# Performance work log

Hardware: AMD Instinct MI355X
Metric: run time of the kernel (lower is better)

Reference implementation:

```python
import jax, jax.numpy as jnp
import numpy as np
from jax import lax

B, T, I, H, N = 8192, 100, 24, 64, 8  # batch, seq_len, input_size, hidden_size, hidden_neurons
H2 = 2 * H


def setup_inputs() -> dict:
    key = jax.random.key(0)
    ks = iter(jax.random.split(key, 80))
    d = {"input_seq": jax.random.normal(next(ks), (B, T, I), jnp.float32)}
    def triple(name, shape):
        d[name + "_mu"] = 0.1 * jax.random.normal(next(ks), shape, jnp.float32)
        d[name + "_rho"] = -6.0 + 0.1 * jax.random.normal(next(ks), shape, jnp.float32)
        d[name + "_eps"] = jax.random.normal(next(ks), shape, jnp.float32)
    # BayesianLSTM params: weight_ih (in, 4H), weight_hh (H, 4H), bias (4H,)
    triple("l1_wih", (I, 4 * H)); triple("l1_whh", (H, 4 * H)); triple("l1_b", (4 * H,))
    triple("l2_wih", (H, 4 * H2)); triple("l2_whh", (H2, 4 * H2)); triple("l2_b", (4 * H2,))
    # BayesianLinear params: weight (out, in), bias (out,)
    triple("fc1_w", (N, H2)); triple("fc1_b", (N,))
    triple("fc2_w", (N, N)); triple("fc2_b", (N,))
    triple("out_w", (1, N)); triple("out_b", (1,))
    return d


def _sample(mu, rho, eps):
    # blitz reparameterization: sigma = log1p(exp(rho))
    return mu + jnp.log1p(jnp.exp(rho)) * eps


def _lstm(x, wih, whh, b):
    # x: [B, T, in]; returns full hidden sequence [B, T, Hn]; gate order i,f,g,o
    Hn = whh.shape[0]
    xg = jnp.einsum('bti,ig->btg', x, wih) + b  # precompute input projection
    def step(carry, xg_t):
        h, c = carry
        gates = xg_t + h @ whh
        i, f, g, o = jnp.split(gates, 4, axis=-1)
        c = jax.nn.sigmoid(f) * c + jax.nn.sigmoid(i) * jnp.tanh(g)
        h = jax.nn.sigmoid(o) * jnp.tanh(c)
        return (h, c), h
    h0 = jnp.zeros((x.shape[0], Hn), x.dtype)
    _, hs = lax.scan(step, (h0, h0), jnp.swapaxes(xg, 0, 1))
    return jnp.swapaxes(hs, 0, 1)


def _forward(input_seq,
             l1_wih_mu, l1_wih_rho, l1_wih_eps, l1_whh_mu, l1_whh_rho, l1_whh_eps,
             l1_b_mu, l1_b_rho, l1_b_eps,
             l2_wih_mu, l2_wih_rho, l2_wih_eps, l2_whh_mu, l2_whh_rho, l2_whh_eps,
             l2_b_mu, l2_b_rho, l2_b_eps,
             fc1_w_mu, fc1_w_rho, fc1_w_eps, fc1_b_mu, fc1_b_rho, fc1_b_eps,
             fc2_w_mu, fc2_w_rho, fc2_w_eps, fc2_b_mu, fc2_b_rho, fc2_b_eps,
             out_w_mu, out_w_rho, out_w_eps, out_b_mu, out_b_rho, out_b_eps):
    w1i = _sample(l1_wih_mu, l1_wih_rho, l1_wih_eps)
    w1h = _sample(l1_whh_mu, l1_whh_rho, l1_whh_eps)
    b1 = _sample(l1_b_mu, l1_b_rho, l1_b_eps)
    w2i = _sample(l2_wih_mu, l2_wih_rho, l2_wih_eps)
    w2h = _sample(l2_whh_mu, l2_whh_rho, l2_whh_eps)
    b2 = _sample(l2_b_mu, l2_b_rho, l2_b_eps)
    fc1w = _sample(fc1_w_mu, fc1_w_rho, fc1_w_eps); fc1b = _sample(fc1_b_mu, fc1_b_rho, fc1_b_eps)
    fc2w = _sample(fc2_w_mu, fc2_w_rho, fc2_w_eps); fc2b = _sample(fc2_b_mu, fc2_b_rho, fc2_b_eps)
    outw = _sample(out_w_mu, out_w_rho, out_w_eps); outb = _sample(out_b_mu, out_b_rho, out_b_eps)

    h1 = _lstm(input_seq, w1i, w1h, b1)      # [B, T, H]
    h2 = _lstm(h1, w2i, w2h, b2)             # [B, T, 2H]
    out = h2[:, -1, :]                       # [B, 2H]
    x = jax.nn.relu(out @ fc1w.T + fc1b)
    x = jax.nn.relu(x @ fc2w.T + fc2b)
    y = x @ outw.T + outb                    # [B, 1]
    return y.reshape(-1)


def reference(input_seq,
              l1_wih_mu, l1_wih_rho, l1_wih_eps, l1_whh_mu, l1_whh_rho, l1_whh_eps,
              l1_b_mu, l1_b_rho, l1_b_eps,
              l2_wih_mu, l2_wih_rho, l2_wih_eps, l2_whh_mu, l2_whh_rho, l2_whh_eps,
              l2_b_mu, l2_b_rho, l2_b_eps,
              fc1_w_mu, fc1_w_rho, fc1_w_eps, fc1_b_mu, fc1_b_rho, fc1_b_eps,
              fc2_w_mu, fc2_w_rho, fc2_w_eps, fc2_b_mu, fc2_b_rho, fc2_b_eps,
              out_w_mu, out_w_rho, out_w_eps, out_b_mu, out_b_rho, out_b_eps):
    return _forward(input_seq,
                    l1_wih_mu, l1_wih_rho, l1_wih_eps, l1_whh_mu, l1_whh_rho, l1_whh_eps,
                    l1_b_mu, l1_b_rho, l1_b_eps,
                    l2_wih_mu, l2_wih_rho, l2_wih_eps, l2_whh_mu, l2_whh_rho, l2_whh_eps,
                    l2_b_mu, l2_b_rho, l2_b_eps,
                    fc1_w_mu, fc1_w_rho, fc1_w_eps, fc1_b_mu, fc1_b_rho, fc1_b_eps,
                    fc2_w_mu, fc2_w_rho, fc2_w_eps, fc2_b_mu, fc2_b_rho, fc2_b_eps,
                    out_w_mu, out_w_rho, out_w_eps, out_b_mu, out_b_rho, out_b_eps)
```

## Files before the change

kernel.cpp:

```cpp
#include <hip/hip_runtime.h>
#include <math.h>


typedef __attribute__((ext_vector_type(8))) short short8;
typedef __attribute__((ext_vector_type(4))) float f32x4;

#define MFMA16(a, b, c) __builtin_amdgcn_mfma_f32_16x16x32_bf16((a), (b), (c), 0, 0, 0)

#define WS_W1G_OFF 196608
#define WS_WF_OFF  245760

struct SampParams {
  const float* w1i[3]; const float* w1h[3]; const float* b1[3];
  const float* w2i[3]; const float* w2h[3]; const float* b2[3];
  const float* f1w[3]; const float* f1b[3];
  const float* f2w[3]; const float* f2b[3];
  const float* ow[3];  const float* ob[3];
  short* W2S; short* W1G; float* WF;
};

struct LstmParams {
  const float* input;
  const short* W2S; const short* W1G; const float* WF;
  float* out;
};

__device__ __forceinline__ float samp(const float* const q[3], int idx) {
  return q[0][idx] + log1pf(expf(q[1][idx])) * q[2][idx];
}

__device__ __forceinline__ short f2bf(float f) {
  unsigned u = __float_as_uint(f);
  unsigned r = (u + 0x7FFFu + ((u >> 16) & 1u)) >> 16;
  return (short)r;
}

__device__ __forceinline__ float sigf(float x) {
  return __builtin_amdgcn_rcpf(1.0f + __builtin_amdgcn_exp2f(-1.44269504f * x));
}
__device__ __forceinline__ float tanhf_(float x) {
  return 1.0f - 2.0f * __builtin_amdgcn_rcpf(1.0f + __builtin_amdgcn_exp2f(2.88539008f * x));
}

__global__ __launch_bounds__(256) void sample_kernel(SampParams p)
{
  int i = blockIdx.x * 256 + threadIdx.x;
  if (i < 12288) {
    int tid = i & 511, gg = (i >> 9) & 3, kk = i >> 11;
    int quad = (tid >> 4) & 3, col = tid & 15, v0 = (tid >> 6) * 16;
    int c = gg * 128 + v0 + col;
    short8 v;
#pragma unroll
    for (int j = 0; j < 8; ++j) {
      int k = kk * 32 + quad * 8 + j;
      float x = (k < 64) ? samp(p.w2i, k * 512 + c) : samp(p.w2h, (k - 64) * 512 + c);
      v[j] = f2bf(x);
    }
    *(short8*)&p.W2S[i * 8] = v;
  } else if (i < 15360) {
    int u = i - 12288;
    int slice = u >> 8, n = u & 255;
    int k0 = (slice >> 2) * 32 + (slice & 3) * 8;
    short8 v;
#pragma unroll
    for (int j = 0; j < 8; ++j) {
      int k = k0 + j;
      float x = 0.0f;
      if (k < 24)       x = samp(p.w1i, k * 256 + n);
      else if (k >= 32) x = samp(p.w1h, (k - 32) * 256 + n);
      v[j] = f2bf(x);
    }
    *(short8*)&p.W1G[u * 8] = v;
  } else if (i < 17241) {
    int u = i - 15360;
    float x;
    if (u < 256)       x = samp(p.b1,  u);
    else if (u < 768)  x = samp(p.b2,  u - 256);
    else if (u < 1792) x = samp(p.f1w, u - 768);
    else if (u < 1856) x = samp(p.f2w, u - 1792);
    else if (u < 1864) x = samp(p.f1b, u - 1856);
    else if (u < 1872) x = samp(p.f2b, u - 1864);
    else if (u < 1880) x = samp(p.ow,  u - 1872);
    else               x = samp(p.ob,  0);
    p.WF[u] = x;
  }
}


__global__ __launch_bounds__(512, 2)
void blstm_kernel(LstmParams p)
{
  __shared__ __align__(16) unsigned char pool[79872];
  short* const W1L = (short*)pool;
  short* const A1b = (short*)(pool + 49152);
  short* const A2b = (short*)(pool + 62464);

  const int tid  = threadIdx.x;
  const int w    = tid >> 6;
  const int l    = tid & 63;
  const int quad = l >> 4;
  const int col  = l & 15;
  const int b0   = blockIdx.x * 32;

  const int wq = w & 3;
  const int mh = w >> 2;
  const int v0 = w * 16;

  const short8* const W2v = (const short8*)p.W2S;
  short8 w2r[24];
#pragma unroll
  for (int f = 0; f < 24; ++f) w2r[f] = W2v[f * 512 + tid];

#pragma unroll
  for (int r = 0; r < 6; ++r) {
    short8 v = *(const short8*)&p.W1G[(r * 512 + tid) * 8];
    *(short8*)&W1L[(r * 512 + tid) * 8] = v;
  }

  float b1v[4], b2v[4];
#pragma unroll
  for (int g = 0; g < 4; ++g) b1v[g] = p.WF[g * 64 + wq * 16 + col];
#pragma unroll
  for (int g = 0; g < 4; ++g) b2v[g] = p.WF[256 + g * 128 + v0 + col];

  for (int i = tid; i < 6656; i += 512) A1b[i] = 0;
  for (int i = tid; i < 8704; i += 512) A2b[i] = 0;
  __syncthreads();

  int xr = 0, xi = 0;
  const float* xptr = p.input;
  if (tid < 384) {
    int e = tid * 2; xr = e / 24; xi = e - xr * 24;
    const float* base = p.input + (size_t)(b0 + xr) * 2400 + xi;
    float2 xv = *(const float2*)base;
    unsigned pk = (unsigned)(unsigned short)f2bf(xv.x)
                | ((unsigned)(unsigned short)f2bf(xv.y) << 16);
    *(unsigned*)&A1b[xr * 104 + xi] = pk;
    xptr = base + 24;
  }
  __syncthreads();

  f32x4 c1 = {0.f, 0.f, 0.f, 0.f};
  f32x4 c2[2]; c2[0] = c1; c2[1] = c1;
  float hf2[2][4];

  const int a1rd = (mh * 16 + col) * 104;

  for (int j = 0; j <= 100; ++j) {
    const int pb = j & 1;
    const short* const A1r = A1b + pb * 3328;
    const short* const A2r = A2b + pb * 4352;
    short* const A1w = A1b + (pb ^ 1) * 3328;
    short* const A2w = A2b + (pb ^ 1) * 4352;

    const bool do_x = (j <= 98) && (tid < 384);
    float2 xv;
    if (do_x) xv = *(const float2*)xptr;

    short8 aA0 = *(const short8*)&A1r[a1rd +      quad * 8];
    short8 aA1 = *(const short8*)&A1r[a1rd + 32 + quad * 8];
    short8 aA2 = *(const short8*)&A1r[a1rd + 64 + quad * 8];
    f32x4 g1[4];
#pragma unroll
    for (int g = 0; g < 4; ++g) {
      f32x4 acc = (f32x4){b1v[g], b1v[g], b1v[g], b1v[g]};
      acc = MFMA16(aA0, *(const short8*)&W1L[(((0 * 4 + quad) << 8) + g * 64 + wq * 16 + col) * 8], acc);
      acc = MFMA16(aA1, *(const short8*)&W1L[(((1 * 4 + quad) << 8) + g * 64 + wq * 16 + col) * 8], acc);
      acc = MFMA16(aA2, *(const short8*)&W1L[(((2 * 4 + quad) << 8) + g * 64 + wq * 16 + col) * 8], acc);
      g1[g] = acc;
    }

    {
      int u = wq * 16 + col;
#pragma unroll
      for (int i = 0; i < 4; ++i) {
        float iv = sigf(g1[0][i]);
        float fv = sigf(g1[1][i]);
        float gv = tanhf_(g1[2][i]);
        float ov = sigf(g1[3][i]);
        float cn = fv * c1[i] + iv * gv;
        c1[i] = cn;
        A1w[(mh * 16 + quad * 4 + i) * 104 + 32 + u] = f2bf(ov * tanhf_(cn));
      }
    }
    if (do_x) {
      unsigned pk = (unsigned)(unsigned short)f2bf(xv.x)
                  | ((unsigned)(unsigned short)f2bf(xv.y) << 16);
      *(unsigned*)&A1w[xr * 104 + xi] = pk;
    }

    f32x4 g2[2][4];
#pragma unroll
    for (int g = 0; g < 4; ++g) {
      g2[0][g] = (f32x4){b2v[g], b2v[g], b2v[g], b2v[g]};
      g2[1][g] = g2[0][g];
    }
#pragma unroll
    for (int kk = 0; kk < 6; ++kk) {
      short8 a0, a1f;
      if (kk < 2) {
        a0  = *(const short8*)&A1r[      col  * 104 + 32 + kk * 32 + quad * 8];
        a1f = *(const short8*)&A1r[(16 + col) * 104 + 32 + kk * 32 + quad * 8];
      } else {
        int o = (kk - 2) * 32 + quad * 8;
        a0  = *(const short8*)&A2r[      col  * 136 + o];
        a1f = *(const short8*)&A2r[(16 + col) * 136 + o];
      }
#pragma unroll
      for (int g = 0; g < 4; ++g) {
        g2[0][g] = MFMA16(a0,  w2r[kk * 4 + g], g2[0][g]);
        g2[1][g] = MFMA16(a1f, w2r[kk * 4 + g], g2[1][g]);
      }
    }

    if (j) {
      int u2 = v0 + col;
#pragma unroll
      for (int mi = 0; mi < 2; ++mi)
#pragma unroll
        for (int i = 0; i < 4; ++i) {
          float iv = sigf(g2[mi][0][i]);
          float fv = sigf(g2[mi][1][i]);
          float gv = tanhf_(g2[mi][2][i]);
          float ov = sigf(g2[mi][3][i]);
          float cn = fv * c2[mi][i] + iv * gv;
          c2[mi][i] = cn;
          float hv = ov * tanhf_(cn);
          hf2[mi][i] = hv;
          A2w[(mi * 16 + quad * 4 + i) * 136 + u2] = f2bf(hv);
        }
    }
    __syncthreads();
    xptr += 24;
  }

  float* const H2   = (float*)pool;
  float* const FC1W = (float*)(pool + 16896);
  float* const FC2W = (float*)(pool + 20992);
  float* const FB1  = (float*)(pool + 21248);
  float* const FB2  = (float*)(pool + 21280);
  float* const OWp  = (float*)(pool + 21312);
  float* const OBp  = (float*)(pool + 21344);
  float* const X1   = (float*)(pool + 21376);
  float* const X2   = (float*)(pool + 22400);

  {
    int u2 = v0 + col;
#pragma unroll
    for (int mi = 0; mi < 2; ++mi)
#pragma unroll
      for (int i = 0; i < 4; ++i) {
        int row = mi * 16 + quad * 4 + i;
        H2[row * 132 + u2] = hf2[mi][i];
      }
  }
  for (int i = tid; i < 1024; i += 512) FC1W[i] = p.WF[768 + i];
  if (tid < 64)               FC2W[tid]     = p.WF[1792 + tid];
  if (tid >= 64 && tid < 72)  FB1[tid - 64] = p.WF[1856 + tid - 64];
  if (tid >= 72 && tid < 80)  FB2[tid - 72] = p.WF[1864 + tid - 72];
  if (tid >= 80 && tid < 88)  OWp[tid - 80] = p.WF[1872 + tid - 80];
  if (tid == 88)              OBp[0]        = p.WF[1880];
  __syncthreads();

  if (tid < 256) {
    int row = tid >> 3, o = tid & 7;
    float s = FB1[o];
#pragma unroll 8
    for (int k = 0; k < 128; ++k) s += H2[row * 132 + k] * FC1W[o * 128 + k];
    X1[tid] = fmaxf(s, 0.0f);
  }
  __syncthreads();
  if (tid < 256) {
    int row = tid >> 3, o = tid & 7;
    float s = FB2[o];
#pragma unroll
    for (int k = 0; k < 8; ++k) s += X1[row * 8 + k] * FC2W[o * 8 + k];
    X2[tid] = fmaxf(s, 0.0f);
  }
  __syncthreads();
  if (tid < 32) {
    float s = OBp[0];
#pragma unroll
    for (int k = 0; k < 8; ++k) s += X2[tid * 8 + k] * OWp[k];
    p.out[b0 + tid] = s;
  }
}

extern "C" void kernel_launch(void* const* d_in, const int* in_sizes, int n_in,
                              void* d_out, int out_size, void* d_ws, size_t ws_size,
                              hipStream_t stream)
{
  (void)in_sizes; (void)n_in; (void)ws_size; (void)out_size;

  SampParams sp;
  const float** grp[12] = { sp.w1i, sp.w1h, sp.b1, sp.w2i, sp.w2h, sp.b2,
                            sp.f1w, sp.f1b, sp.f2w, sp.f2b, sp.ow, sp.ob };
  int idx = 1;
  for (int t = 0; t < 12; ++t)
    for (int j = 0; j < 3; ++j)
      grp[t][j] = (const float*)d_in[idx++];
  sp.W2S = (short*)d_ws;
  sp.W1G = (short*)((char*)d_ws + WS_W1G_OFF);
  sp.WF  = (float*)((char*)d_ws + WS_WF_OFF);

  LstmParams bp;
  bp.input = (const float*)d_in[0];
  bp.W2S = (const short*)d_ws;
  bp.W1G = (const short*)((char*)d_ws + WS_W1G_OFF);
  bp.WF  = (const float*)((char*)d_ws + WS_WF_OFF);
  bp.out = (float*)d_out;

  sample_kernel<<<dim3(68), dim3(256), 0, stream>>>(sp);
  blstm_kernel<<<dim3(256), dim3(512), 0, stream>>>(bp);
}
```

Baseline: 416.2 us.

## Fuse LSTM gate rcps, use hardware bf16 pack, stagger per-wave layer order

Replaces separate sigmoid/tanh reciprocals with a fused element routine that shares one reciprocal per pair of gates, cutting transcendental ops per cell. Swaps the manual bf16 rounding for the v_cvt_pk_bf16_f32 instruction. Half the waves now run layer 2 before layer 1 so MFMA and transcendental-heavy phases from different waves interleave, and the layer-2 MFMA block gets raised scheduling priority. Also uses a fast exp2/log softplus in the sampling kernel. Multiplying two (1+exp) terms can overflow to infinity for large gate magnitudes, which may turn paired gate outputs into NaN or zero.

```diff
diff --git a/kernel.cpp b/kernel.cpp
--- a/kernel.cpp
+++ b/kernel.cpp
@@ -25,8 +25,13 @@
   float* out;
 };
 
+__device__ __forceinline__ float softplus_fast(float x) {
+  float e = __builtin_amdgcn_exp2f(1.44269504f * x);
+  return 0.69314718f * __builtin_amdgcn_logf(1.0f + e);
+}
+
 __device__ __forceinline__ float samp(const float* const q[3], int idx) {
-  return q[0][idx] + log1pf(expf(q[1][idx])) * q[2][idx];
+  return q[0][idx] + softplus_fast(q[1][idx]) * q[2][idx];
 }
 
 __device__ __forceinline__ short f2bf(float f) {
@@ -35,11 +40,28 @@
   return (short)r;
 }
 
-__device__ __forceinline__ float sigf(float x) {
-  return __builtin_amdgcn_rcpf(1.0f + __builtin_amdgcn_exp2f(-1.44269504f * x));
-}
-__device__ __forceinline__ float tanhf_(float x) {
-  return 1.0f - 2.0f * __builtin_amdgcn_rcpf(1.0f + __builtin_amdgcn_exp2f(2.88539008f * x));
+__device__ __forceinline__ unsigned cvt_pk_bf16(float lo, float hi) {
+  unsigned r;
+  asm("v_cvt_pk_bf16_f32 %0, %1, %2" : "=v"(r) : "v"(lo), "v"(hi));
+  return r;
+}
+
+__device__ __forceinline__ void lstm_elem(float gi, float gf, float gg, float go,
+                                          float& c, float& h) {
+  float A = 1.0f + __builtin_amdgcn_exp2f(-1.44269504f * gi);
+  float B = 1.0f + __builtin_amdgcn_exp2f(-1.44269504f * gf);
+  float r = __builtin_amdgcn_rcpf(A * B);
+  float si = r * B;
+  float sf = r * A;
+  float C = 1.0f + __builtin_amdgcn_exp2f(2.88539008f * gg);
+  float D = 1.0f + __builtin_amdgcn_exp2f(-1.44269504f * go);
+  float r2 = __builtin_amdgcn_rcpf(C * D);
+  float tg = 1.0f - 2.0f * (r2 * D);
+  float so = r2 * C;
+  float cn = sf * c + si * tg;
+  c = cn;
+  float E = 1.0f + __builtin_amdgcn_exp2f(2.88539008f * cn);
+  h = so * (1.0f - 2.0f * __builtin_amdgcn_rcpf(E));
 }
 
 __global__ __launch_bounds__(256) void sample_kernel(SampParams p)
@@ -133,15 +155,13 @@
     int e = tid * 2; xr = e / 24; xi = e - xr * 24;
     const float* base = p.input + (size_t)(b0 + xr) * 2400 + xi;
     float2 xv = *(const float2*)base;
-    unsigned pk = (unsigned)(unsigned short)f2bf(xv.x)
-                | ((unsigned)(unsigned short)f2bf(xv.y) << 16);
-    *(unsigned*)&A1b[xr * 104 + xi] = pk;
+    *(unsigned*)&A1b[xr * 104 + xi] = cvt_pk_bf16(xv.x, xv.y);
     xptr = base + 24;
   }
   __syncthreads();
 
-  f32x4 c1 = {0.f, 0.f, 0.f, 0.f};
-  f32x4 c2[2]; c2[0] = c1; c2[1] = c1;
+  float c1a[4]  = {0.f, 0.f, 0.f, 0.f};
+  float c2a[2][4] = {{0.f,0.f,0.f,0.f},{0.f,0.f,0.f,0.f}};
   float hf2[2][4];
 
   const int a1rd = (mh * 16 + col) * 104;
@@ -157,79 +177,87 @@
     float2 xv;
     if (do_x) xv = *(const float2*)xptr;
 
-    short8 aA0 = *(const short8*)&A1r[a1rd +      quad * 8];
-    short8 aA1 = *(const short8*)&A1r[a1rd + 32 + quad * 8];
-    short8 aA2 = *(const short8*)&A1r[a1rd + 64 + quad * 8];
-    f32x4 g1[4];
-#pragma unroll
-    for (int g = 0; g < 4; ++g) {
-      f32x4 acc = (f32x4){b1v[g], b1v[g], b1v[g], b1v[g]};
-      acc = MFMA16(aA0, *(const short8*)&W1L[(((0 * 4 + quad) << 8) + g * 64 + wq * 16 + col) * 8], acc);
-      acc = MFMA16(aA1, *(const short8*)&W1L[(((1 * 4 + quad) << 8) + g * 64 + wq * 16 + col) * 8], acc);
-      acc = MFMA16(aA2, *(const short8*)&W1L[(((2 * 4 + quad) << 8) + g * 64 + wq * 16 + col) * 8], acc);
-      g1[g] = acc;
-    }
-
-    {
-      int u = wq * 16 + col;
-#pragma unroll
-      for (int i = 0; i < 4; ++i) {
-        float iv = sigf(g1[0][i]);
-        float fv = sigf(g1[1][i]);
-        float gv = tanhf_(g1[2][i]);
-        float ov = sigf(g1[3][i]);
-        float cn = fv * c1[i] + iv * gv;
-        c1[i] = cn;
-        A1w[(mh * 16 + quad * 4 + i) * 104 + 32 + u] = f2bf(ov * tanhf_(cn));
-      }
-    }
-    if (do_x) {
-      unsigned pk = (unsigned)(unsigned short)f2bf(xv.x)
-                  | ((unsigned)(unsigned short)f2bf(xv.y) << 16);
-      *(unsigned*)&A1w[xr * 104 + xi] = pk;
-    }
-
-    f32x4 g2[2][4];
-#pragma unroll
-    for (int g = 0; g < 4; ++g) {
-      g2[0][g] = (f32x4){b2v[g], b2v[g], b2v[g], b2v[g]};
-      g2[1][g] = g2[0][g];
-    }
-#pragma unroll
-    for (int kk = 0; kk < 6; ++kk) {
-      short8 a0, a1f;
-      if (kk < 2) {
-        a0  = *(const short8*)&A1r[      col  * 104 + 32 + kk * 32 + quad * 8];
-        a1f = *(const short8*)&A1r[(16 + col) * 104 + 32 + kk * 32 + quad * 8];
-      } else {
-        int o = (kk - 2) * 32 + quad * 8;
-        a0  = *(const short8*)&A2r[      col  * 136 + o];
-        a1f = *(const short8*)&A2r[(16 + col) * 136 + o];
-      }
+    auto do_l1 = [&]() {
+      short8 aA0 = *(const short8*)&A1r[a1rd +      quad * 8];
+      short8 aA1 = *(const short8*)&A1r[a1rd + 32 + quad * 8];
+      short8 aA2 = *(const short8*)&A1r[a1rd + 64 + quad * 8];
+      f32x4 g1[4];
 #pragma unroll
       for (int g = 0; g < 4; ++g) {
-        g2[0][g] = MFMA16(a0,  w2r[kk * 4 + g], g2[0][g]);
-        g2[1][g] = MFMA16(a1f, w2r[kk * 4 + g], g2[1][g]);
-      }
-    }
-
-    if (j) {
-      int u2 = v0 + col;
-#pragma unroll
-      for (int mi = 0; mi < 2; ++mi)
-#pragma unroll
-        for (int i = 0; i < 4; ++i) {
-          float iv = sigf(g2[mi][0][i]);
-          float fv = sigf(g2[mi][1][i]);
-          float gv = tanhf_(g2[mi][2][i]);
-          float ov = sigf(g2[mi][3][i]);
-          float cn = fv * c2[mi][i] + iv * gv;
-          c2[mi][i] = cn;
-          float hv = ov * tanhf_(cn);
-          hf2[mi][i] = hv;
-          A2w[(mi * 16 + quad * 4 + i) * 136 + u2] = f2bf(hv);
+        f32x4 acc = (f32x4){b1v[g], b1v[g], b1v[g], b1v[g]};
+        acc = MFMA16(aA0, *(const short8*)&W1L[(((0 * 4 + quad) << 8) + g * 64 + wq * 16 + col) * 8], acc);
+        acc = MFMA16(aA1, *(const short8*)&W1L[(((1 * 4 + quad) << 8) + g * 64 + wq * 16 + col) * 8], acc);
+        acc = MFMA16(aA2, *(const short8*)&W1L[(((2 * 4 + quad) << 8) + g * 64 + wq * 16 + col) * 8], acc);
+        g1[g] = acc;
+      }
+      float h1v[4];
+#pragma unroll
+      for (int i = 0; i < 4; ++i)
+        lstm_elem(g1[0][i], g1[1][i], g1[2][i], g1[3][i], c1a[i], h1v[i]);
+      {
+        int base = (mh * 16 + quad * 4) * 104 + 32 + wq * 16 + col;
+        unsigned pkA = cvt_pk_bf16(h1v[0], h1v[1]);
+        unsigned pkB = cvt_pk_bf16(h1v[2], h1v[3]);
+        A1w[base]       = (short)pkA;
+        A1w[base + 104] = (short)(pkA >> 16);
+        A1w[base + 208] = (short)pkB;
+        A1w[base + 312] = (short)(pkB >> 16);
+      }
+      if (do_x)
+        *(unsigned*)&A1w[xr * 104 + xi] = cvt_pk_bf16(xv.x, xv.y);
+    };
+
+    auto do_l2 = [&]() {
+      f32x4 g2[2][4];
+#pragma unroll
+      for (int g = 0; g < 4; ++g) {
+        g2[0][g] = (f32x4){b2v[g], b2v[g], b2v[g], b2v[g]};
+        g2[1][g] = g2[0][g];
+      }
+      __builtin_amdgcn_s_setprio(1);
+#pragma unroll
+      for (int kk = 0; kk < 6; ++kk) {
+        short8 a0, a1f;
+        if (kk < 2) {
+          a0  = *(const short8*)&A1r[      col  * 104 + 32 + kk * 32 + quad * 8];
+          a1f = *(const short8*)&A1r[(16 + col) * 104 + 32 + kk * 32 + quad * 8];
+        } else {
+          int o = (kk - 2) * 32 + quad * 8;
+          a0  = *(const short8*)&A2r[      col  * 136 + o];
+          a1f = *(const short8*)&A2r[(16 + col) * 136 + o];
         }
-    }
+#pragma unroll
+        for (int g = 0; g < 4; ++g) {
+          g2[0][g] = MFMA16(a0,  w2r[kk * 4 + g], g2[0][g]);
+          g2[1][g] = MFMA16(a1f, w2r[kk * 4 + g], g2[1][g]);
+        }
+      }
+      __builtin_amdgcn_s_setprio(0);
+      if (j) {
+        int u2 = v0 + col;
+#pragma unroll
+        for (int mi = 0; mi < 2; ++mi) {
+          float hv[4];
+#pragma unroll
+          for (int i = 0; i < 4; ++i) {
+            lstm_elem(g2[mi][0][i], g2[mi][1][i], g2[mi][2][i], g2[mi][3][i],
+                      c2a[mi][i], hv[i]);
+            hf2[mi][i] = hv[i];
+          }
+          unsigned pkA = cvt_pk_bf16(hv[0], hv[1]);
+          unsigned pkB = cvt_pk_bf16(hv[2], hv[3]);
+          int base = (mi * 16 + quad * 4) * 136 + u2;
+          A2w[base]       = (short)pkA;
+          A2w[base + 136] = (short)(pkA >> 16);
+          A2w[base + 272] = (short)pkB;
+          A2w[base + 408] = (short)(pkB >> 16);
+        }
+      }
+    };
+
+    if (w < 4) { do_l1(); do_l2(); }
+    else       { do_l2(); do_l1(); }
+
     __syncthreads();
     xptr += 24;
   }
```

New measurement: 433.4 us. +4.1%, slower.
